# Kernel optimization log

Hardware: AMD Instinct MI355X
Metric: run time of the kernel (lower is better)

## Reference

```python
import jax, jax.numpy as jnp
import numpy as np
from jax import lax


def _conv1x1(x, w):
    # x: [B,Cin,H,W], w: [Cout,Cin]
    return jnp.einsum('bchw,oc->bohw', x, w)


def _dwconv(x, w, pad):
    # depthwise conv, w: [C,1,k,k]
    return lax.conv_general_dilated(
        x, w, window_strides=(1, 1), padding=[(pad, pad), (pad, pad)],
        dimension_numbers=('NCHW', 'OIHW', 'NCHW'),
        feature_group_count=w.shape[0])


def _l2norm(x, axis=-1, eps=1e-12):
    n = jnp.sqrt(jnp.sum(x * x, axis=axis, keepdims=True))
    return x / jnp.maximum(n, eps)


def _topk_masked_softmax(attn, k):
    # attn: [B,H,C,C]; keep top-k per row, -inf elsewhere, softmax
    B, H, C, _ = attn.shape
    flat = attn.reshape(B * H * C, C)
    vals, idx = lax.top_k(flat, k)
    rows = jnp.arange(flat.shape[0])[:, None]
    scat = jnp.full_like(flat, -jnp.inf).at[rows, idx].set(vals)
    return jax.nn.softmax(scat, axis=-1).reshape(B, H, C, C)


def setup_inputs() -> dict:
    key = jax.random.key(0)
    ks = jax.random.split(key, 7)
    dim, heads = 384, 8
    x = jax.random.normal(ks[0], (2, dim, 128, 128), jnp.float32)
    s = 0.02
    w_qkv = jax.random.normal(ks[1], (dim * 3, dim), jnp.float32) * s
    w_dw3 = jax.random.normal(ks[2], (dim * 3, 1, 3, 3), jnp.float32) * s
    w_dw5 = jax.random.normal(ks[3], (dim * 3, 1, 5, 5), jnp.float32) * s
    w_dw7 = jax.random.normal(ks[4], (dim * 3, 1, 7, 7), jnp.float32) * s
    w_pconv = jax.random.normal(ks[5], (dim * 3, dim * 9), jnp.float32) * s
    w_proj = jax.random.normal(ks[6], (dim, dim), jnp.float32) * s
    temperature = jnp.ones((heads, 1, 1), jnp.float32)
    attn_scales = jnp.full((3,), 0.2, jnp.float32)
    return {"x": x, "w_qkv": w_qkv, "w_dw3": w_dw3, "w_dw5": w_dw5,
            "w_dw7": w_dw7, "w_pconv": w_pconv, "w_proj": w_proj,
            "temperature": temperature, "attn_scales": attn_scales}


def reference(x, w_qkv, w_dw3, w_dw5, w_dw7, w_pconv, w_proj, temperature, attn_scales):
    b, c, h, w = x.shape
    heads = temperature.shape[0]
    base = _conv1x1(x, w_qkv)                       # [B,3C,H,W]
    qkv = jnp.concatenate([_dwconv(base, w_dw3, 1),
                           _dwconv(base, w_dw5, 2),
                           _dwconv(base, w_dw7, 3)], axis=1)  # [B,9C,H,W]
    qkv = _conv1x1(qkv, w_pconv)                    # [B,3C,H,W]
    q, k, v = jnp.split(qkv, 3, axis=1)
    def heads_split(t):
        return t.reshape(b, heads, c // heads, h * w)
    q, k, v = heads_split(q), heads_split(k), heads_split(v)
    q = _l2norm(q)
    k = _l2norm(k)
    attn = jnp.einsum('bhcn,bhdn->bhcd', q, k) * temperature  # [B,H,C,C]
    C = q.shape[2]
    out = jnp.zeros_like(v)
    for i, top_k in enumerate([int(C / 2), int(C * 2 / 3), int(C * 3 / 4)]):
        a = _topk_masked_softmax(attn, top_k)
        out = out + attn_scales[i] * jnp.einsum('bhcd,bhdn->bhcn', a, v)
    out = out.reshape(b, c, h, w)
    return _conv1x1(out, w_proj)
```

## Files before the change

### kernel.cpp

```cpp
#include <hip/hip_runtime.h>
#include <hip/hip_bf16.h>
#include <stdint.h>

typedef __attribute__((ext_vector_type(4))) float f32x4;
typedef __attribute__((ext_vector_type(8))) short s16x8;
typedef __attribute__((ext_vector_type(4))) short s16x4;
typedef __attribute__((ext_vector_type(8))) _Float16 f16x8;

__device__ __forceinline__ float bf2f(unsigned short u){
  union { unsigned int i; float f; } v; v.i = ((unsigned int)u) << 16; return v.f;
}
__device__ __forceinline__ unsigned short f2bf(float f){
  union { float f; unsigned int i; } v; v.f = f;
  unsigned int r = v.i + 0x7fffu + ((v.i >> 16) & 1u);
  return (unsigned short)(r >> 16);
}
__device__ __forceinline__ unsigned short f2h(float f){
  union { _Float16 h; unsigned short u; } v; v.h = (_Float16)f; return v.u;
}
__device__ __forceinline__ void gload_lds16(const void* g, void* l){
  __builtin_amdgcn_global_load_lds(
      (const __attribute__((address_space(1))) void*)g,
      (__attribute__((address_space(3))) void*)l, 16, 0, 0);
}

__device__ __forceinline__ void swz_decode(int id, int mtiles, int& m0, int& n0){
  const int xcd = id & 7;
  const int r = id >> 3;
  m0 = (r % mtiles) * 128;
  n0 = ((r / mtiles)*8 + xcd) * 128;
}

template<int MODE>
__global__ __launch_bounds__(256, 2)
void k_gemm(const unsigned short* __restrict__ A, const unsigned short* __restrict__ Bt,
            void* __restrict__ Cp, int M, int N, int K, int ldb){
  __shared__ unsigned short sm[16384];
  const int tid = threadIdx.x;
  const int lane = tid & 63;
  const int wid = tid >> 6;
  int m0, n0;
  swz_decode(blockIdx.x, M >> 7, m0, n0);
  const int wm = wid & 1;
  const int wn = wid >> 1;

  f32x4 acc[4][4];
  #pragma unroll
  for (int i = 0; i < 4; ++i)
    #pragma unroll
    for (int j = 0; j < 4; ++j)
      acc[i][j] = (f32x4){0.f, 0.f, 0.f, 0.f};

  const unsigned short* ga[4];
  const unsigned short* gb[4];
  unsigned short* la[4];
  unsigned short* lb[4];
  #pragma unroll
  for (int i = 0; i < 4; ++i){
    const int row = (wid*4 + i)*8 + (lane >> 3);
    const int slot = (lane & 7) ^ (row & 7);
    ga[i] = A  + (size_t)(m0 + row)*K   + slot*8;
    gb[i] = Bt + (size_t)(n0 + row)*ldb + slot*8;
    la[i] = &sm[(wid*4 + i)*512];
    lb[i] = &sm[8192 + (wid*4 + i)*512];
  }

  const int nkt = K >> 6;
  for (int kt = 0; kt < nkt; ++kt){
    if (kt) __syncthreads();
    #pragma unroll
    for (int i = 0; i < 4; ++i){
      gload_lds16(ga[i] + kt*64, la[i]);
      gload_lds16(gb[i] + kt*64, lb[i]);
    }
    __syncthreads();
    #pragma unroll
    for (int kk = 0; kk < 2; ++kk){
      s16x8 af[4], bfv[4];
      #pragma unroll
      for (int im = 0; im < 4; ++im){
        const int row = wm*64 + im*16 + (lane & 15);
        const int s = ((kk*4) | (lane >> 4)) ^ (row & 7);
        af[im] = *(const s16x8*)((const char*)sm + row*128 + s*16);
      }
      #pragma unroll
      for (int in = 0; in < 4; ++in){
        const int row = wn*64 + in*16 + (lane & 15);
        const int s = ((kk*4) | (lane >> 4)) ^ (row & 7);
        bfv[in] = *(const s16x8*)((const char*)sm + 16384 + row*128 + s*16);
      }
      #pragma unroll
      for (int im = 0; im < 4; ++im)
        #pragma unroll
        for (int in = 0; in < 4; ++in)
          acc[im][in] = __builtin_amdgcn_mfma_f32_16x16x32_bf16(af[im], bfv[in], acc[im][in], 0, 0, 0);
    }
  }

  if (MODE == 2){
    float* C = (float*)Cp;
    #pragma unroll
    for (int im = 0; im < 4; ++im){
      const int m = m0 + wm*64 + im*16 + (lane >> 4)*4;
      #pragma unroll
      for (int in = 0; in < 4; ++in){
        const int n = n0 + wn*64 + in*16 + (lane & 15);
        #pragma unroll
        for (int r = 0; r < 4; ++r)
          C[(size_t)(m + r)*N + n] = acc[im][in][r];
      }
    }
    return;
  }

  float* ep = (float*)sm;
  for (int p = 0; p < 2; ++p){
    __syncthreads();
    if (wn == p){
      #pragma unroll
      for (int in = 0; in < 4; ++in){
        const int n2 = in*16 + (lane & 15);
        const int e = (n2 & 7) << 2;
        #pragma unroll
        for (int im = 0; im < 4; ++im){
          const int t = (wm*64 + im*16 + (lane >> 4)*4) >> 2;
          *(f32x4*)(&ep[n2*128 + ((t ^ e) << 2)]) = acc[im][in];
        }
      }
    }
    __syncthreads();
    float* C = (float*)Cp;
    #pragma unroll
    for (int j = 0; j < 8; ++j){
      const int cidx = tid + j*256;
      const int n2 = cidx >> 5, t = cidx & 31;
      const int e = (n2 & 7) << 2;
      const f32x4 v = *(const f32x4*)(&ep[n2*128 + ((t ^ e) << 2)]);
      const int cb = (m0 >> 4) + (t >> 2);
      const int off = (t & 3)*4;
      float* dst = C + ((size_t)cb*16384 + (n0 + p*64 + n2))*16 + off;
      *(f32x4*)dst = v;
    }
  }
}

__global__ __launch_bounds__(256, 2)
void k_gemm_f9(const unsigned short* __restrict__ Wp16, const unsigned short* __restrict__ Bt,
               float* __restrict__ qkT, unsigned short* __restrict__ vT, int startPx, int cpx){
  __shared__ unsigned short sm[24576];
  const int tid = threadIdx.x;
  const int lane = tid & 63;
  const int wid = tid >> 6;
  const int xcd = blockIdx.x & 7;
  const int rr = blockIdx.x >> 3;
  const int m0 = (rr % 9) * 128;
  const int n0 = ((rr/9)*8 + xcd) * 256;
  const bool isV = (m0 >= 768);
  const int wm = wid & 1;
  const int wn = wid >> 1;

  f32x4 acc[4][8];
  #pragma unroll
  for (int i = 0; i < 4; ++i)
    #pragma unroll
    for (int j = 0; j < 8; ++j)
      acc[i][j] = (f32x4){0.f, 0.f, 0.f, 0.f};

  const unsigned short* ga[4];
  unsigned short* la[4];
  int brow[8], bslot[8];
  unsigned short* lb[8];
  #pragma unroll
  for (int i = 0; i < 4; ++i){
    const int row = (wid*4 + i)*8 + (lane >> 3);
    const int slot = (lane & 7) ^ (row & 7);
    ga[i] = Wp16 + (size_t)(m0 + row)*3456 + slot*8;
    la[i] = &sm[(wid*4 + i)*512];
  }
  #pragma unroll
  for (int i = 0; i < 8; ++i){
    const int row = (wid*8 + i)*8 + (lane >> 3);
    const int slot = (lane & 7) ^ (row & 7);
    brow[i] = n0 + row; bslot[i] = slot;
    lb[i] = &sm[8192 + (wid*8 + i)*512];
  }

  for (int kt = 0; kt < 54; ++kt){
    if (kt) __syncthreads();
    #pragma unroll
    for (int i = 0; i < 4; ++i)
      gload_lds16(ga[i] + kt*64, la[i]);
    #pragma unroll
    for (int i = 0; i < 8; ++i){
      const int k0 = kt*64 + bslot[i]*8;
      const int cb = k0 / 48;
      const int off = k0 - cb*48;
      gload_lds16(Bt + ((size_t)cb*cpx + brow[i])*48 + off, lb[i]);
    }
    __syncthreads();
    #pragma unroll
    for (int kk = 0; kk < 2; ++kk){
      f16x8 af[4], bfv[8];
      #pragma unroll
      for (int im = 0; im < 4; ++im){
        const int row = wm*64 + im*16 + (lane & 15);
        const int s = ((kk*4) | (lane >> 4)) ^ (row & 7);
        af[im] = *(const f16x8*)((const char*)sm + row*128 + s*16);
      }
      #pragma unroll
      for (int in = 0; in < 8; ++in){
        const int row = wn*128 + in*16 + (lane & 15);
        const int s = ((kk*4) | (lane >> 4)) ^ (row & 7);
        bfv[in] = *(const f16x8*)((const char*)sm + 16384 + row*128 + s*16);
      }
      #pragma unroll
      for (int im = 0; im < 4; ++im)
        #pragma unroll
        for (int in = 0; in < 8; ++in)
          acc[im][in] = __builtin_amdgcn_mfma_f32_16x16x32_f16(af[im], bfv[in], acc[im][in], 0, 0, 0);
    }
  }

  float* ep = (float*)sm;
  for (int p = 0; p < 4; ++p){
    __syncthreads();
    if (wn == (p >> 1)){
      #pragma unroll
      for (int in2 = 0; in2 < 4; ++in2){
        const int n2 = in2*16 + (lane & 15);
        const int e = (n2 & 7) << 2;
        #pragma unroll
        for (int im = 0; im < 4; ++im){
          const int t = (wm*64 + im*16 + (lane >> 4)*4) >> 2;
          *(f32x4*)(&ep[n2*128 + ((t ^ e) << 2)]) = acc[im][(p & 1)*4 + in2];
        }
      }
    }
    __syncthreads();
    if (!isV){
      #pragma unroll
      for (int j = 0; j < 8; ++j){
        const int cidx = tid + j*256;
        const int n2 = cidx >> 5, t = cidx & 31;
        const int e = (n2 & 7) << 2;
        const f32x4 v = *(const f32x4*)(&ep[n2*128 + ((t ^ e) << 2)]);
        *(f32x4*)(qkT + (size_t)(n0 + p*64 + n2)*768 + m0 + t*4) = v;
      }
    } else {
      #pragma unroll
      for (int j = 0; j < 4; ++j){
        const int cidx = tid + j*256;
        const int n2 = cidx >> 4, u2 = cidx & 15;
        const int e = (n2 & 7) << 2;
        const f32x4 lo = *(const f32x4*)(&ep[n2*128 + (((2*u2    ) ^ e) << 2)]);
        const f32x4 hi = *(const f32x4*)(&ep[n2*128 + (((2*u2 + 1) ^ e) << 2)]);
        s16x8 o;
        #pragma unroll
        for (int q = 0; q < 4; ++q){ o[q] = (short)f2bf(lo[q]); o[4 + q] = (short)f2bf(hi[q]); }
        *(s16x8*)(vT + (size_t)(startPx + n0 + p*64 + n2)*384 + (m0 - 768) + u2*8) = o;
      }
    }
  }
}

__global__ __launch_bounds__(256)
void k_transpose_xhl(const float* __restrict__ x, unsigned short* __restrict__ xT2){
  __shared__ float lds[64*65];
  const int tid = threadIdx.x;
  const int px0 = blockIdx.x*64;
  const int c0 = blockIdx.y*64;
  #pragma unroll
  for (int it = 0; it < 4; ++it){
    const int idx = tid + it*256;
    const int cl = idx >> 4, col = idx & 15;
    const f32x4 v = *(const f32x4*)(x + (size_t)(c0 + cl)*16384 + px0 + col*4);
    float* d = &lds[cl*65 + col*4];
    d[0] = v[0]; d[1] = v[1]; d[2] = v[2]; d[3] = v[3];
  }
  __syncthreads();
  #pragma unroll
  for (int it = 0; it < 2; ++it){
    const int idx = tid + it*256;
    const int pl = idx >> 3, cg = idx & 7;
    s16x8 h, l;
    #pragma unroll
    for (int j = 0; j < 8; ++j){
      const float v = lds[(cg*8 + j)*65 + pl];
      const unsigned short hb = f2bf(v);
      h[j] = (short)hb;
      l[j] = (short)f2bf(v - bf2f(hb));
    }
    unsigned short* o = xT2 + (size_t)(px0 + pl)*1152 + c0 + cg*8;
    *(s16x8*)(o)       = h;
    *(s16x8*)(o + 384) = l;
    *(s16x8*)(o + 768) = h;
  }
}

__global__ __launch_bounds__(512, 1)
void k_dwconv(const float* __restrict__ base2,
              const float* __restrict__ w3, const float* __restrict__ w5,
              const float* __restrict__ w7, unsigned short* __restrict__ dwT2,
              int y_base_rows, int start_px, int cpx){
  __shared__ float tile[10*72*16];
  __shared__ float wl[16*83];
  const int tid = threadIdx.x;
  const int cb = blockIdx.x;
  const int c0 = cb*16;
  const int y0 = y_base_rows + blockIdx.y*4;
  const int x0 = blockIdx.z*64;

  for (int u = tid; u < 16*83; u += 512){
    float wv;
    if (u < 144){ const int tap = u >> 4, cl = u & 15; wv = w3[(c0 + cl)*9 + tap]; }
    else if (u < 544){ const int v2 = u - 144; const int tap = v2/16, cl = v2%16; wv = w5[(c0 + cl)*25 + tap]; }
    else { const int v2 = u - 544; const int tap = v2/16, cl = v2%16; wv = w7[(c0 + cl)*49 + tap]; }
    wl[u] = wv;
  }
  const float* bb = base2 + (size_t)cb*16384*16;
  for (int u = tid; u < 2880; u += 512){
    const int r = u / 288;
    const int rem = u % 288;
    const int xig = rem >> 2;
    const int cq = rem & 3;
    const int y = y0 + r - 3;
    const int xg = x0 + xig - 3;
    f32x4 v = {0.f,0.f,0.f,0.f};
    if ((unsigned)y < 128u && (unsigned)xg < 128u)
      v = *(const f32x4*)(bb + (size_t)(y*128 + xg)*16 + cq*4);
    *(f32x4*)(&tile[(r*72 + xig)*16 + cq*4]) = v;
  }
  __syncthreads();

  const int cq = tid & 3;
  const int xl = (tid >> 2) & 63;
  const int rh = tid >> 8;
  const float* w3t = wl;
  const float* w5t = wl + 144;
  const float* w7t = wl + 544;

  f32x4 a3[2], a5[2], a7[2];
  #pragma unroll
  for (int r = 0; r < 2; ++r){
    a3[r] = (f32x4){0.f,0.f,0.f,0.f};
    a5[r] = (f32x4){0.f,0.f,0.f,0.f};
    a7[r] = (f32x4){0.f,0.f,0.f,0.f};
  }
  #pragma unroll
  for (int dy = 0; dy < 7; ++dy){
    #pragma unroll
    for (int dx = 0; dx < 7; ++dx){
      const f32x4 w7v = *(const f32x4*)(&w7t[(dy*7 + dx)*16 + cq*4]);
      const bool in5 = (dy >= 1 && dy <= 5 && dx >= 1 && dx <= 5);
      const bool in3 = (dy >= 2 && dy <= 4 && dx >= 2 && dx <= 4);
      f32x4 w5v = {0.f,0.f,0.f,0.f}, w3v = {0.f,0.f,0.f,0.f};
      if (in5) w5v = *(const f32x4*)(&w5t[((dy - 1)*5 + (dx - 1))*16 + cq*4]);
      if (in3) w3v = *(const f32x4*)(&w3t[((dy - 2)*3 + (dx - 2))*16 + cq*4]);
      #pragma unroll
      for (int r = 0; r < 2; ++r){
        const f32x4 f = *(const f32x4*)(&tile[((rh*2 + r + dy)*72 + (xl + dx))*16 + cq*4]);
        a7[r] += f*w7v;
        if (in5) a5[r] += f*w5v;
        if (in3) a3[r] += f*w3v;
      }
    }
  }

  #pragma unroll
  for (int r = 0; r < 2; ++r){
    const int p = (y0 + rh*2 + r)*128 + x0 + xl;
    unsigned short* ob = dwT2 + ((size_t)cb*cpx + (p - start_px))*48 + cq*4;
    s16x4 h3, h5, h7;
    #pragma unroll
    for (int j = 0; j < 4; ++j){
      h3[j] = (short)f2h(a3[r][j]);
      h5[j] = (short)f2h(a5[r][j]);
      h7[j] = (short)f2h(a7[r][j]);
    }
    *(s16x4*)(ob)      = h3;
    *(s16x4*)(ob + 16) = h5;
    *(s16x4*)(ob + 32) = h7;
  }
}

__global__ __launch_bounds__(256, 2)
void k_attn_partial2(const float* __restrict__ qkT, float* __restrict__ part, int slotBase){
  __shared__ float qk[16*772];
  const int tid = threadIdx.x;
  const int slot = blockIdx.x;
  const int c0 = tid & 15;
  const int d0 = tid >> 4;

  float acc[8][3][3];
  #pragma unroll
  for (int h = 0; h < 8; ++h)
    #pragma unroll
    for (int i = 0; i < 3; ++i)
      #pragma unroll
      for (int j = 0; j < 3; ++j)
        acc[h][i][j] = 0.f;
  float ssq0 = 0.f, ssq1 = 0.f, ssq2 = 0.f;
  const int ch = tid*3;

  for (int sub = 0; sub < 4; ++sub){
    __syncthreads();
    const int pb = slot*64 + sub*16;
    #pragma unroll
    for (int it = 0; it < 12; ++it){
      const int idx = tid + it*256;
      const int px = idx / 192, s = idx % 192;
      *(f32x4*)(&qk[px*772 + s*4]) = *(const f32x4*)(qkT + (size_t)(pb + px)*768 + s*4);
    }
    __syncthreads();
    for (int px = 0; px < 16; ++px){
      const float* row = &qk[px*772];
      #pragma unroll
      for (int h = 0; h < 8; ++h){
        const float q0 = row[h*48 + c0*3 + 0];
        const float q1 = row[h*48 + c0*3 + 1];
        const float q2 = row[h*48 + c0*3 + 2];
        const float k0 = row[384 + h*48 + d0*3 + 0];
        const float k1 = row[384 + h*48 + d0*3 + 1];
        const float k2 = row[384 + h*48 + d0*3 + 2];
        acc[h][0][0] += q0*k0; acc[h][0][1] += q0*k1; acc[h][0][2] += q0*k2;
        acc[h][1][0] += q1*k0; acc[h][1][1] += q1*k1; acc[h][1][2] += q1*k2;
        acc[h][2][0] += q2*k0; acc[h][2][1] += q2*k1; acc[h][2][2] += q2*k2;
      }
      ssq0 += row[ch]*row[ch];
      ssq1 += row[ch + 1]*row[ch + 1];
      ssq2 += row[ch + 2]*row[ch + 2];
    }
  }

  #pragma unroll
  for (int h = 0; h < 8; ++h){
    float* pp = part + ((size_t)h*256 + slotBase + slot)*2400;
    #pragma unroll
    for (int i = 0; i < 3; ++i)
      #pragma unroll
      for (int j = 0; j < 3; ++j)
        pp[(c0*3 + i)*48 + d0*3 + j] = acc[h][i][j];
  }
  {
    const int hh = (ch < 384) ? (ch / 48) : ((ch - 384) / 48);
    const int cc = (ch < 384) ? (ch % 48) : (48 + ((ch - 384) % 48));
    float* pp = part + ((size_t)hh*256 + slotBase + slot)*2400 + 2304 + cc;
    pp[0] = ssq0; pp[1] = ssq1; pp[2] = ssq2;
  }
}

__global__ __launch_bounds__(256)
void k_attn_combine(const float* __restrict__ part, const float* __restrict__ temp,
                    const float* __restrict__ scales, float* __restrict__ Acomb){
  __shared__ float att[288];
  const int tid = threadIdx.x;
  const int rg = blockIdx.x;
  const int h = blockIdx.y;
  const int r0 = rg*4;
  for (int u = tid; u < 288; u += 256){
    const int off = (u < 192) ? ((r0 + u/48)*48 + (u % 48)) : (2304 + (u - 192));
    float s = 0.f;
    const float* pb = part + (size_t)h*256*2400 + off;
    for (int c2 = 0; c2 < 256; ++c2) s += pb[c2*2400];
    att[u] = s;
  }
  __syncthreads();
  const int w = tid >> 6;
  const int lane = tid & 63;
  const int c = r0 + w;
  const int d = lane;
  const float tmp = temp[h];
  float v;
  if (d < 48){
    const float nq = fmaxf(sqrtf(att[192 + c]), 1e-12f);
    const float nk = fmaxf(sqrtf(att[240 + d]), 1e-12f);
    v = att[w*48 + d] / (nq*nk) * tmp;
  } else v = -3.0e38f;
  float m = v;
  #pragma unroll
  for (int s = 32; s; s >>= 1) m = fmaxf(m, __shfl_xor(m, s, 64));
  int rk = 0;
  for (int l = 0; l < 48; ++l){
    const float vl = __shfl(v, l, 64);
    rk += ((vl > v) || (vl == v && l < d)) ? 1 : 0;
  }
  const float e = (d < 48) ? expf(v - m) : 0.f;
  float e0 = (rk < 24) ? e : 0.f;
  float e1 = (rk < 32) ? e : 0.f;
  float e2 = (rk < 36) ? e : 0.f;
  #pragma unroll
  for (int s = 32; s; s >>= 1){
    e0 += __shfl_xor(e0, s, 64);
    e1 += __shfl_xor(e1, s, 64);
    e2 += __shfl_xor(e2, s, 64);
  }
  const float wgt = e*(((rk < 24) ? scales[0]/e0 : 0.f)
                     + ((rk < 32) ? scales[1]/e1 : 0.f)
                     + ((rk < 36) ? scales[2]/e2 : 0.f));
  if (d < 48) Acomb[((size_t)h*48 + c)*48 + d] = wgt;
}

__global__ __launch_bounds__(256, 2)
void k_av(const unsigned short* __restrict__ vT, const float* __restrict__ Acomb,
          unsigned short* __restrict__ outT){
  __shared__ float As[48*49];
  __shared__ float vs[64*48];
  const int tid = threadIdx.x;
  const int pc = blockIdx.x;
  const int h = blockIdx.y;
  for (int u = tid; u < 2304; u += 256)
    As[(u/48)*49 + (u%48)] = Acomb[(size_t)h*2304 + u];
  const int q = tid & 3;
  const int pl = tid >> 2;
  for (int st = 0; st < 4; ++st){
    __syncthreads();
    const int pb = pc*256 + st*64;
    #pragma unroll
    for (int it = 0; it < 2; ++it){
      const int u = tid + it*256;
      if (u < 384){
        const int p = u / 6, sg = u % 6;
        const s16x8 v8 = *(const s16x8*)(vT + (size_t)(pb + p)*384 + h*48 + sg*8);
        float* d = &vs[p*48 + sg*8];
        #pragma unroll
        for (int j = 0; j < 8; ++j) d[j] = bf2f((unsigned short)v8[j]);
      }
    }
    __syncthreads();
    float a[12];
    #pragma unroll
    for (int i = 0; i < 12; ++i) a[i] = 0.f;
    for (int d = 0; d < 48; ++d){
      const float vv = vs[pl*48 + d];
      #pragma unroll
      for (int i = 0; i < 12; ++i) a[i] += As[(q*12 + i)*49 + d]*vv;
    }
    unsigned short* ob = outT + (size_t)(pb + pl)*384 + h*48 + q*12;
    #pragma unroll
    for (int g = 0; g < 3; ++g){
      s16x4 o;
      #pragma unroll
      for (int j = 0; j < 4; ++j) o[j] = (short)f2bf(a[g*4 + j]);
      *(s16x4*)(ob + g*4) = o;
    }
  }
}

__global__ __launch_bounds__(256)
void k_f32_to_bf16(const float* __restrict__ in, unsigned short* __restrict__ out, int n4){
  const int i = blockIdx.x*256 + threadIdx.x;
  if (i < n4){
    const f32x4 v = *(const f32x4*)(in + (size_t)i*4);
    s16x4 o;
    #pragma unroll
    for (int j = 0; j < 4; ++j) o[j] = (short)f2bf(v[j]);
    *(s16x4*)(out + (size_t)i*4) = o;
  }
}
__global__ __launch_bounds__(256)
void k_prep_wqkv(const float* __restrict__ w, unsigned short* __restrict__ A){
  const int i = blockIdx.x*256 + threadIdx.x;
  const int o = i / 384, c = i % 384;
  const float v = w[i];
  const unsigned short hi = f2bf(v);
  const unsigned short lo = f2bf(v - bf2f(hi));
  unsigned short* r = A + (size_t)o*1152;
  r[c] = hi; r[384 + c] = hi; r[768 + c] = lo;
}
__global__ __launch_bounds__(256)
void k_prep_wp16(const float* __restrict__ w, unsigned short* __restrict__ wp16){
  const int i = blockIdx.x*256 + threadIdx.x;
  const int o = i / 3456, k3 = i % 3456;
  const int cbl = k3 / 48, r2 = k3 % 48, br = r2 / 16, cl = r2 % 16;
  wp16[(size_t)o*3456 + k3] = f2h(w[(size_t)o*3456 + br*1152 + cbl*16 + cl]);
}

extern "C" void kernel_launch(void* const* d_in, const int* in_sizes, int n_in,
                              void* d_out, int out_size, void* d_ws, size_t ws_size,
                              hipStream_t stream){
  const float* x         = (const float*)d_in[0];
  const float* w_qkv     = (const float*)d_in[1];
  const float* w_dw3     = (const float*)d_in[2];
  const float* w_dw5     = (const float*)d_in[3];
  const float* w_dw7     = (const float*)d_in[4];
  const float* w_pconv   = (const float*)d_in[5];
  const float* w_proj    = (const float*)d_in[6];
  const float* temperature = (const float*)d_in[7];
  const float* attn_scales = (const float*)d_in[8];
  float* out = (float*)d_out;
  char* ws = (char*)d_ws;
  const size_t MiB = (size_t)1 << 20;

  unsigned short* Aqkv  = (unsigned short*)(ws);
  unsigned short* Wp16  = (unsigned short*)(ws + 3*MiB);
  unsigned short* Wproj = (unsigned short*)(ws + 11*MiB);
  unsigned short* vT    = (unsigned short*)(ws + 12*MiB);
  char* tailp = ws + (ws_size - 33*MiB);
  float*          part  = (float*)tailp;
  float*          Acomb = (float*)(tailp + 20*MiB);
  unsigned short* outT  = (unsigned short*)(tailp + 21*MiB);

  float*          base2;
  float*          qkTc;
  unsigned short* dwT2;
  unsigned short* xT2;
  int units;
  if (ws_size >= 237*MiB){
    base2 = (float*)(ws + 24*MiB);
    qkTc  = (float*)(ws + 24*MiB);
    dwT2  = (unsigned short*)(ws + 96*MiB);
    xT2   = (unsigned short*)(ws + 96*MiB);
    units = 16;
  } else {
    base2 = (float*)(ws + 24*MiB);
    long long avail = (long long)ws_size - (long long)(96 + 33)*MiB;
    units = (int)(avail / (1024LL*768*4 + 1024LL*3456*2));
    if (units > 16) units = 16;
    units &= ~1;
    if (units < 2) units = 2;
    qkTc = (float*)(ws + 96*MiB);
    dwT2 = (unsigned short*)(ws + 96*MiB + (size_t)units*3*MiB);
    xT2  = (unsigned short*)(ws + 96*MiB);
  }

  k_prep_wqkv<<<dim3(1728), dim3(256), 0, stream>>>(w_qkv, Aqkv);
  k_prep_wp16<<<dim3(15552), dim3(256), 0, stream>>>(w_pconv, Wp16);
  k_f32_to_bf16<<<dim3(144), dim3(256), 0, stream>>>(w_proj, Wproj, 36864);

  for (int b = 0; b < 2; ++b){
    const float* xb = x + (size_t)b*384*16384;
    float* outb = out + (size_t)b*384*16384;
    k_transpose_xhl<<<dim3(256, 6), dim3(256), 0, stream>>>(xb, xT2);
    k_gemm<4><<<dim3(1152), dim3(256), 0, stream>>>(Aqkv, xT2, base2, 1152, 16384, 1152, 1152);
    for (int u0 = 0; u0 < 16; u0 += units){
      const int cu = (units < 16 - u0) ? units : (16 - u0);
      const int start = u0*1024, cpx = cu*1024;
      k_dwconv<<<dim3(72, cu*2, 2), dim3(512), 0, stream>>>(base2, w_dw3, w_dw5, w_dw7,
                                                            dwT2, start/128, start, cpx);
      k_gemm_f9<<<dim3((cpx/256)*9), dim3(256), 0, stream>>>(Wp16, dwT2, qkTc, vT, start, cpx);
      k_attn_partial2<<<dim3(cpx/64), dim3(256), 0, stream>>>(qkTc, part, start/64);
    }
    k_attn_combine<<<dim3(12, 8), dim3(256), 0, stream>>>(part, temperature, attn_scales, Acomb);
    k_av<<<dim3(64, 8), dim3(256), 0, stream>>>(vT, Acomb, outT);
    k_gemm<2><<<dim3(128*3), dim3(256), 0, stream>>>(Wproj, outT, outb, 384, 16384, 384, 384);
  }
  (void)in_sizes; (void)n_in; (void)out_size; (void)ws_size;
}
```

Baseline: 982.7 us.

## Widen qkv GEMM tile and store dwconv output pixel-major for f9 GEMM

Adds a dedicated qkv projection kernel with a 128x256 tile (8 N-fragments per wave), halving the block count and reusing A-tile loads across more columns. The generic GEMM is reduced to its direct-store epilogue. The depthwise conv output is now laid out pixel-major with a 3456-element row stride, so the pconv GEMM loads B with plain strided pointers instead of per-iteration divide-by-48 address math. This trades more accumulator registers per thread and a different write pattern in dwconv for simpler, more contiguous GEMM loads.

```diff
diff --git a/kernel.cpp b/kernel.cpp
--- a/kernel.cpp
+++ b/kernel.cpp
@@ -97,39 +97,108 @@
     }
   }
 
-  if (MODE == 2){
-    float* C = (float*)Cp;
-    #pragma unroll
-    for (int im = 0; im < 4; ++im){
-      const int m = m0 + wm*64 + im*16 + (lane >> 4)*4;
-      #pragma unroll
-      for (int in = 0; in < 4; ++in){
-        const int n = n0 + wn*64 + in*16 + (lane & 15);
+  float* C = (float*)Cp;
+  #pragma unroll
+  for (int im = 0; im < 4; ++im){
+    const int m = m0 + wm*64 + im*16 + (lane >> 4)*4;
+    #pragma unroll
+    for (int in = 0; in < 4; ++in){
+      const int n = n0 + wn*64 + in*16 + (lane & 15);
+      #pragma unroll
+      for (int r = 0; r < 4; ++r)
+        C[(size_t)(m + r)*N + n] = acc[im][in][r];
+    }
+  }
+}
+
+__global__ __launch_bounds__(256, 2)
+void k_gemm4w(const unsigned short* __restrict__ A, const unsigned short* __restrict__ Bt,
+              float* __restrict__ C){
+  __shared__ unsigned short sm[24576];
+  const int tid = threadIdx.x;
+  const int lane = tid & 63;
+  const int wid = tid >> 6;
+  const int xcd = blockIdx.x & 7;
+  const int rr = blockIdx.x >> 3;
+  const int m0 = (rr % 9) * 128;
+  const int n0 = ((rr/9)*8 + xcd) * 256;
+  const int wm = wid & 1;
+  const int wn = wid >> 1;
+
+  f32x4 acc[4][8];
+  #pragma unroll
+  for (int i = 0; i < 4; ++i)
+    #pragma unroll
+    for (int j = 0; j < 8; ++j)
+      acc[i][j] = (f32x4){0.f, 0.f, 0.f, 0.f};
+
+  const unsigned short* ga[4];
+  unsigned short* la[4];
+  const unsigned short* gb[8];
+  unsigned short* lb[8];
+  #pragma unroll
+  for (int i = 0; i < 4; ++i){
+    const int row = (wid*4 + i)*8 + (lane >> 3);
+    const int slot = (lane & 7) ^ (row & 7);
+    ga[i] = A + (size_t)(m0 + row)*1152 + slot*8;
+    la[i] = &sm[(wid*4 + i)*512];
+  }
+  #pragma unroll
+  for (int i = 0; i < 8; ++i){
+    const int row = (wid*8 + i)*8 + (lane >> 3);
+    const int slot = (lane & 7) ^ (row & 7);
+    gb[i] = Bt + (size_t)(n0 + row)*1152 + slot*8;
+    lb[i] = &sm[8192 + (wid*8 + i)*512];
+  }
+
+  for (int kt = 0; kt < 18; ++kt){
+    if (kt) __syncthreads();
+    #pragma unroll
+    for (int i = 0; i < 4; ++i)
+      gload_lds16(ga[i] + kt*64, la[i]);
+    #pragma unroll
+    for (int i = 0; i < 8; ++i)
+      gload_lds16(gb[i] + kt*64, lb[i]);
+    __syncthreads();
+    #pragma unroll
+    for (int kk = 0; kk < 2; ++kk){
+      s16x8 af[4], bfv[8];
+      #pragma unroll
+      for (int im = 0; im < 4; ++im){
+        const int row = wm*64 + im*16 + (lane & 15);
+        const int s = ((kk*4) | (lane >> 4)) ^ (row & 7);
+        af[im] = *(const s16x8*)((const char*)sm + row*128 + s*16);
+      }
+      #pragma unroll
+      for (int in = 0; in < 8; ++in){
+        const int row = wn*128 + in*16 + (lane & 15);
+        const int s = ((kk*4) | (lane >> 4)) ^ (row & 7);
+        bfv[in] = *(const s16x8*)((const char*)sm + 16384 + row*128 + s*16);
+      }
+      #pragma unroll
+      for (int im = 0; im < 4; ++im)
         #pragma unroll
-        for (int r = 0; r < 4; ++r)
-          C[(size_t)(m + r)*N + n] = acc[im][in][r];
-      }
-    }
-    return;
+        for (int in = 0; in < 8; ++in)
+          acc[im][in] = __builtin_amdgcn_mfma_f32_16x16x32_bf16(af[im], bfv[in], acc[im][in], 0, 0, 0);
+    }
   }
 
   float* ep = (float*)sm;
-  for (int p = 0; p < 2; ++p){
-    __syncthreads();
-    if (wn == p){
-      #pragma unroll
-      for (int in = 0; in < 4; ++in){
-        const int n2 = in*16 + (lane & 15);
+  for (int p = 0; p < 4; ++p){
+    __syncthreads();
+    if (wn == (p >> 1)){
+      #pragma unroll
+      for (int in2 = 0; in2 < 4; ++in2){
+        const int n2 = in2*16 + (lane & 15);
         const int e = (n2 & 7) << 2;
         #pragma unroll
         for (int im = 0; im < 4; ++im){
           const int t = (wm*64 + im*16 + (lane >> 4)*4) >> 2;
-          *(f32x4*)(&ep[n2*128 + ((t ^ e) << 2)]) = acc[im][in];
+          *(f32x4*)(&ep[n2*128 + ((t ^ e) << 2)]) = acc[im][(p & 1)*4 + in2];
         }
       }
     }
     __syncthreads();
-    float* C = (float*)Cp;
     #pragma unroll
     for (int j = 0; j < 8; ++j){
       const int cidx = tid + j*256;
@@ -168,7 +237,7 @@
 
   const unsigned short* ga[4];
   unsigned short* la[4];
-  int brow[8], bslot[8];
+  const unsigned short* gb[8];
   unsigned short* lb[8];
   #pragma unroll
   for (int i = 0; i < 4; ++i){
@@ -181,7 +250,7 @@
   for (int i = 0; i < 8; ++i){
     const int row = (wid*8 + i)*8 + (lane >> 3);
     const int slot = (lane & 7) ^ (row & 7);
-    brow[i] = n0 + row; bslot[i] = slot;
+    gb[i] = Bt + (size_t)(n0 + row)*3456 + slot*8;
     lb[i] = &sm[8192 + (wid*8 + i)*512];
   }
 
@@ -191,12 +260,8 @@
     for (int i = 0; i < 4; ++i)
       gload_lds16(ga[i] + kt*64, la[i]);
     #pragma unroll
-    for (int i = 0; i < 8; ++i){
-      const int k0 = kt*64 + bslot[i]*8;
-      const int cb = k0 / 48;
-      const int off = k0 - cb*48;
-      gload_lds16(Bt + ((size_t)cb*cpx + brow[i])*48 + off, lb[i]);
-    }
+    for (int i = 0; i < 8; ++i)
+      gload_lds16(gb[i] + kt*64, lb[i]);
     __syncthreads();
     #pragma unroll
     for (int kk = 0; kk < 2; ++kk){
@@ -369,7 +434,7 @@
   #pragma unroll
   for (int r = 0; r < 2; ++r){
     const int p = (y0 + rh*2 + r)*128 + x0 + xl;
-    unsigned short* ob = dwT2 + ((size_t)cb*cpx + (p - start_px))*48 + cq*4;
+    unsigned short* ob = dwT2 + (size_t)(p - start_px)*3456 + cb*48 + cq*4;
     s16x4 h3, h5, h7;
     #pragma unroll
     for (int j = 0; j < 4; ++j){
@@ -631,7 +696,7 @@
     const float* xb = x + (size_t)b*384*16384;
     float* outb = out + (size_t)b*384*16384;
     k_transpose_xhl<<<dim3(256, 6), dim3(256), 0, stream>>>(xb, xT2);
-    k_gemm<4><<<dim3(1152), dim3(256), 0, stream>>>(Aqkv, xT2, base2, 1152, 16384, 1152, 1152);
+    k_gemm4w<<<dim3(576), dim3(256), 0, stream>>>(Aqkv, xT2, base2);
     for (int u0 = 0; u0 < 16; u0 += units){
       const int cu = (units < 16 - u0) ? units : (16 - u0);
       const int start = u0*1024, cpx = cu*1024;
```

Measured after the change: 973.3 us. No clear change (-1.0%).
